# Kernel optimization log

Hardware: AMD Instinct MI355X
Metric: run time of the kernel (lower is better)

Reference implementation:

```python
import jax, jax.numpy as jnp
import numpy as np

def setup_inputs() -> dict:
    key = jax.random.key(0)
    k1, k2, k3, k4, k5 = jax.random.split(key, 5)
    vocab, embed, hidden = 32000, 1024, 1024
    batch, src_len = 64, 512
    src = jax.random.randint(k1, (batch, src_len), 0, vocab)
    emb_table = jax.random.normal(k2, (vocab, embed), dtype=jnp.float32)
    # xavier_uniform bounds
    bx = float(np.sqrt(6.0 / (embed + hidden)))
    bh = float(np.sqrt(6.0 / (hidden + hidden)))
    W_xh = jax.random.uniform(k3, (hidden, embed), minval=-bx, maxval=bx, dtype=jnp.float32)
    b_xh = jax.random.uniform(k4, (hidden,), minval=-1.0/np.sqrt(embed), maxval=1.0/np.sqrt(embed), dtype=jnp.float32)
    W_hh = jax.random.uniform(k5, (hidden, hidden), minval=-bh, maxval=bh, dtype=jnp.float32)
    return {"src": src, "emb_table": emb_table, "W_xh": W_xh, "b_xh": b_xh, "W_hh": W_hh}

def reference(src, emb_table, W_xh, b_xh, W_hh):
    # embedded: (batch, src_len, embed)
    embedded = emb_table[src]
    # precompute input projection for all timesteps: (batch, src_len, hidden)
    x_proj = jnp.einsum('bte,he->bth', embedded, W_xh) + b_xh
    batch = src.shape[0]
    hidden = W_hh.shape[0]
    h0 = jnp.zeros((batch, hidden), dtype=jnp.float32)

    def step(h, x_t):
        h_new = jnp.tanh(x_t + h @ W_hh.T)
        return h_new, None

    # scan over time: x_proj transposed to (src_len, batch, hidden)
    h_final, _ = jax.lax.scan(step, h0, jnp.swapaxes(x_proj, 0, 1))
    return h_final
```

## Files before the change

### kernel.cpp

```cpp
#include <hip/hip_runtime.h>
#include <hip/hip_fp16.h>

typedef _Float16 half8 __attribute__((ext_vector_type(8)));
typedef float floatx4 __attribute__((ext_vector_type(4)));

#define HBUF_BYTES (2ull * 16 * 1024 * 8)
#define CTL_BYTES  (32ull * 1024)
#define XP_OFF     (HBUF_BYTES + CTL_BYTES)
#define XP_BYTES   (512ull * 64 * 1024 * 2)
#define FLAG_STRIDE 16

union pack4 { unsigned long long u; _Float16 h[4]; };

__device__ inline half8 cvt8(const float4 a, const float4 b) {
    half8 r;
    r[0] = (_Float16)a.x; r[1] = (_Float16)a.y; r[2] = (_Float16)a.z; r[3] = (_Float16)a.w;
    r[4] = (_Float16)b.x; r[5] = (_Float16)b.y; r[6] = (_Float16)b.z; r[7] = (_Float16)b.w;
    return r;
}

__global__ __launch_bounds__(256) void xproj_kernel(
    const int* __restrict__ src, const float* __restrict__ emb,
    const float* __restrict__ Wxh, const float* __restrict__ bxh,
    _Float16* __restrict__ xp)
{
    __shared__ _Float16 As[128][40];
    __shared__ _Float16 Bs[128][40];

    const int tid  = threadIdx.x;
    const int lane = tid & 63;
    const int w    = tid >> 6;
    const int m15  = lane & 15;
    const int quad = lane >> 4;
    const int bid  = blockIdx.x;
    const int bn   = bid & 7;
    const int bm   = bid >> 3;
    const int m0   = bm * 128, n0 = bn * 128;
    const int wm   = w & 1, wn = w >> 1;

    const int  srow = tid >> 1;
    const int  scol = (tid & 1) * 16;
    const long arow = (long)src[m0 + srow] * 1024;
    const float* abase = emb + arow + scol;
    const float* bbase = Wxh + (long)(n0 + srow) * 1024 + scol;

    floatx4 zero4 = {0.f, 0.f, 0.f, 0.f};
    floatx4 acc[4][4];
#pragma unroll
    for (int mt = 0; mt < 4; mt++)
#pragma unroll
        for (int nt = 0; nt < 4; nt++) acc[mt][nt] = zero4;

    for (int k0 = 0; k0 < 1024; k0 += 32) {
        __syncthreads();
        float4 a0 = *(const float4*)(abase + k0);
        float4 a1 = *(const float4*)(abase + k0 + 4);
        float4 a2 = *(const float4*)(abase + k0 + 8);
        float4 a3 = *(const float4*)(abase + k0 + 12);
        float4 b0 = *(const float4*)(bbase + k0);
        float4 b1 = *(const float4*)(bbase + k0 + 4);
        float4 b2 = *(const float4*)(bbase + k0 + 8);
        float4 b3 = *(const float4*)(bbase + k0 + 12);
        *(half8*)&As[srow][scol]     = cvt8(a0, a1);
        *(half8*)&As[srow][scol + 8] = cvt8(a2, a3);
        *(half8*)&Bs[srow][scol]     = cvt8(b0, b1);
        *(half8*)&Bs[srow][scol + 8] = cvt8(b2, b3);
        __syncthreads();

        half8 af[4], bf[4];
#pragma unroll
        for (int mt = 0; mt < 4; mt++)
            af[mt] = *(const half8*)&As[wm * 64 + mt * 16 + m15][quad * 8];
#pragma unroll
        for (int nt = 0; nt < 4; nt++)
            bf[nt] = *(const half8*)&Bs[wn * 64 + nt * 16 + m15][quad * 8];
#pragma unroll
        for (int mt = 0; mt < 4; mt++)
#pragma unroll
            for (int nt = 0; nt < 4; nt++)
                acc[mt][nt] = __builtin_amdgcn_mfma_f32_16x16x32_f16(
                    af[mt], bf[nt], acc[mt][nt], 0, 0, 0);
    }

#pragma unroll
    for (int nt = 0; nt < 4; nt++) {
        const int n = n0 + wn * 64 + nt * 16 + m15;
        const float bias = bxh[n];
#pragma unroll
        for (int mt = 0; mt < 4; mt++) {
            const int mrow = m0 + wm * 64 + mt * 16 + quad * 4;
#pragma unroll
            for (int r = 0; r < 4; r++) {
                const int m = mrow + r;
                const int b = m >> 9;
                const int t = m & 511;
                xp[((long)t * 64 + b) * 1024 + n] = (_Float16)(acc[mt][nt][r] + bias);
            }
        }
    }
}

__global__ __launch_bounds__(256, 1) void rnn_kernel(
    const float* __restrict__ Whh, const _Float16* __restrict__ xp,
    unsigned long long* __restrict__ hb, int* __restrict__ flags,
    float* __restrict__ out)
{
    __shared__ _Float16 hstage[16][1032];
    __shared__ floatx4  cred[4][4][64];

    const int tid    = threadIdx.x;
    const int lane   = tid & 63;
    const int w      = tid >> 6;
    const int m15    = lane & 15;
    const int quad   = lane >> 4;
    const int wg     = blockIdx.x;
    const int g      = wg & 15;
    const int member = wg >> 4;
    const int b0     = g * 4;

    for (int i = tid; i < 16 * 1032; i += 256) ((_Float16*)hstage)[i] = (_Float16)0.f;

    half8 Wf[4][8];
#pragma unroll
    for (int nt = 0; nt < 4; nt++) {
        const float* wrow = Whh + (long)(member * 64 + nt * 16 + m15) * 1024
                                + w * 256 + quad * 8;
#pragma unroll
        for (int kk = 0; kk < 8; kk++) {
            float4 lo = *(const float4*)(wrow + kk * 32);
            float4 hi = *(const float4*)(wrow + kk * 32 + 4);
            Wf[nt][kk] = cvt8(lo, hi);
        }
    }
    __syncthreads();

    const int dim = member * 64 + w * 16 + m15;
    float xv[4] = {0.f, 0.f, 0.f, 0.f};
    if (quad == 0) {
#pragma unroll
        for (int r = 0; r < 4; r++)
            xv[r] = (float)xp[((long)0 * 64 + b0 + r) * 1024 + dim];
    }

    int* myflag = flags + (g * 16 + member) * FLAG_STRIDE;
    const int* gflags = flags + g * 16 * FLAG_STRIDE;
    floatx4 zero4 = {0.f, 0.f, 0.f, 0.f};

    for (int t = 0; t < 512; t++) {
        const unsigned long long* hcu = hb + (size_t)(t & 1) * 16384 + (size_t)g * 1024;
        unsigned long long*       hnu = hb + (size_t)((t + 1) & 1) * 16384 + (size_t)g * 1024;

        if (t > 0) {
            if (tid < 16) {
                const int* fw = gflags + tid * FLAG_STRIDE;
                while (__hip_atomic_load(fw, __ATOMIC_RELAXED,
                                         __HIP_MEMORY_SCOPE_AGENT) < t) { }
            }
            __syncthreads();
        }

        {
            unsigned long long v[4];
#pragma unroll
            for (int i = 0; i < 4; i++)
                v[i] = __hip_atomic_load(hcu + tid + 256 * i, __ATOMIC_RELAXED,
                                         __HIP_MEMORY_SCOPE_AGENT);
#pragma unroll
            for (int i = 0; i < 4; i++) {
                pack4 p; p.u = v[i];
                const int d = tid + 256 * i;
#pragma unroll
                for (int b = 0; b < 4; b++) hstage[b][d] = p.h[b];
            }
        }
        __syncthreads();

        floatx4 pacc[4];
#pragma unroll
        for (int nt = 0; nt < 4; nt++) pacc[nt] = zero4;
#pragma unroll
        for (int kk = 0; kk < 8; kk++) {
            half8 a = *(const half8*)&hstage[m15][w * 256 + kk * 32 + quad * 8];
#pragma unroll
            for (int nt = 0; nt < 4; nt++)
                pacc[nt] = __builtin_amdgcn_mfma_f32_16x16x32_f16(
                    a, Wf[nt][kk], pacc[nt], 0, 0, 0);
        }

#pragma unroll
        for (int nt = 0; nt < 4; nt++) cred[w][nt][lane] = pacc[nt];
        __syncthreads();
        floatx4 dsum = cred[0][w][lane];
#pragma unroll
        for (int ww = 1; ww < 4; ww++) dsum += cred[ww][w][lane];

        if (quad == 0) {
            pack4 p;
#pragma unroll
            for (int r = 0; r < 4; r++) {
                float pre  = dsum[r] + xv[r];
                float e    = __expf(2.0f * pre);
                float hval = 1.0f - 2.0f / (e + 1.0f);
                p.h[r] = (_Float16)hval;
                if (t == 511) out[(b0 + r) * 1024 + dim] = hval;
            }
            __hip_atomic_store(hnu + dim, p.u, __ATOMIC_RELAXED,
                               __HIP_MEMORY_SCOPE_AGENT);
        }

        __syncthreads();
        if (tid == 0)
            __hip_atomic_store(myflag, t + 1, __ATOMIC_RELAXED,
                               __HIP_MEMORY_SCOPE_AGENT);

        if (t < 511 && quad == 0) {
#pragma unroll
            for (int r = 0; r < 4; r++)
                xv[r] = (float)xp[((long)(t + 1) * 64 + b0 + r) * 1024 + dim];
        }
    }
}

extern "C" void kernel_launch(void* const* d_in, const int* in_sizes, int n_in,
                              void* d_out, int out_size, void* d_ws, size_t ws_size,
                              hipStream_t stream) {
    const int*   src = (const int*)d_in[0];
    const float* emb = (const float*)d_in[1];
    const float* Wxh = (const float*)d_in[2];
    const float* bxh = (const float*)d_in[3];
    const float* Whh = (const float*)d_in[4];
    float* out = (float*)d_out;

    char* ws = (char*)d_ws;
    unsigned long long* hb = (unsigned long long*)ws;
    int* flags = (int*)(ws + HBUF_BYTES);
    _Float16* xp = (_Float16*)(ws + XP_OFF);

    hipMemsetAsync(ws, 0, HBUF_BYTES + CTL_BYTES, stream);

    hipLaunchKernelGGL(xproj_kernel, dim3(2048), dim3(256), 0, stream,
                       src, emb, Wxh, bxh, xp);

    hipLaunchKernelGGL(rnn_kernel, dim3(256), dim3(256), 0, stream,
                       Whh, xp, hb, flags, out);
}
```

Measured before the change: 1.309 ms.

## Replace per-step flag barrier with parity-tagged hidden-state polling

The separate flag array and its spin-wait plus store handshake are removed. Consumers now spin directly on the hidden-state words until a parity tag, kept in bit 14, matches the expected step. Bit 14 is the top fp16 exponent bit of the first packed element, which is always zero for tanh outputs. This drops one global round trip and two __syncthreads per timestep from the serial recurrence. In exchange, every thread polls global memory, and correctness now depends on the tag bit never being set by real hidden values.

Measured after the change: 1.197 ms. -8.5%, faster.

```diff
diff --git a/kernel.cpp b/kernel.cpp
--- a/kernel.cpp
+++ b/kernel.cpp
@@ -8,7 +8,8 @@
 #define CTL_BYTES  (32ull * 1024)
 #define XP_OFF     (HBUF_BYTES + CTL_BYTES)
 #define XP_BYTES   (512ull * 64 * 1024 * 2)
-#define FLAG_STRIDE 16
+
+#define TAG_BIT    (1ull << 14)
 
 union pack4 { unsigned long long u; _Float16 h[4]; };
 
@@ -102,8 +103,7 @@
 
 __global__ __launch_bounds__(256, 1) void rnn_kernel(
     const float* __restrict__ Whh, const _Float16* __restrict__ xp,
-    unsigned long long* __restrict__ hb, int* __restrict__ flags,
-    float* __restrict__ out)
+    unsigned long long* __restrict__ hb, float* __restrict__ out)
 {
     __shared__ _Float16 hstage[16][1032];
     __shared__ floatx4  cred[4][4][64];
@@ -142,36 +142,31 @@
             xv[r] = (float)xp[((long)0 * 64 + b0 + r) * 1024 + dim];
     }
 
-    int* myflag = flags + (g * 16 + member) * FLAG_STRIDE;
-    const int* gflags = flags + g * 16 * FLAG_STRIDE;
     floatx4 zero4 = {0.f, 0.f, 0.f, 0.f};
 
     for (int t = 0; t < 512; t++) {
         const unsigned long long* hcu = hb + (size_t)(t & 1) * 16384 + (size_t)g * 1024;
         unsigned long long*       hnu = hb + (size_t)((t + 1) & 1) * 16384 + (size_t)g * 1024;
-
-        if (t > 0) {
-            if (tid < 16) {
-                const int* fw = gflags + tid * FLAG_STRIDE;
-                while (__hip_atomic_load(fw, __ATOMIC_RELAXED,
-                                         __HIP_MEMORY_SCOPE_AGENT) < t) { }
-            }
-            __syncthreads();
-        }
-
-        {
-            unsigned long long v[4];
+        const unsigned long long exp_tag = (unsigned long long)(((t + 1) >> 1) & 1) << 14;
+
+        unsigned long long v[4];
+        for (;;) {
+            bool ok = true;
 #pragma unroll
             for (int i = 0; i < 4; i++)
                 v[i] = __hip_atomic_load(hcu + tid + 256 * i, __ATOMIC_RELAXED,
                                          __HIP_MEMORY_SCOPE_AGENT);
 #pragma unroll
-            for (int i = 0; i < 4; i++) {
-                pack4 p; p.u = v[i];
-                const int d = tid + 256 * i;
-#pragma unroll
-                for (int b = 0; b < 4; b++) hstage[b][d] = p.h[b];
-            }
+            for (int i = 0; i < 4; i++)
+                ok &= ((v[i] & TAG_BIT) == exp_tag);
+            if (ok) break;
+        }
+#pragma unroll
+        for (int i = 0; i < 4; i++) {
+            pack4 p; p.u = v[i] & ~TAG_BIT;
+            const int d = tid + 256 * i;
+#pragma unroll
+            for (int b = 0; b < 4; b++) hstage[b][d] = p.h[b];
         }
         __syncthreads();
 
@@ -204,14 +199,13 @@
                 p.h[r] = (_Float16)hval;
                 if (t == 511) out[(b0 + r) * 1024 + dim] = hval;
             }
-            __hip_atomic_store(hnu + dim, p.u, __ATOMIC_RELAXED,
-                               __HIP_MEMORY_SCOPE_AGENT);
-        }
-
-        __syncthreads();
-        if (tid == 0)
-            __hip_atomic_store(myflag, t + 1, __ATOMIC_RELAXED,
-                               __HIP_MEMORY_SCOPE_AGENT);
+            if (t < 511) {
+                const unsigned long long st_tag =
+                    (unsigned long long)(((t + 2) >> 1) & 1) << 14;
+                __hip_atomic_store(hnu + dim, p.u | st_tag, __ATOMIC_RELAXED,
+                                   __HIP_MEMORY_SCOPE_AGENT);
+            }
+        }
 
         if (t < 511 && quad == 0) {
 #pragma unroll
@@ -233,14 +227,13 @@
 
     char* ws = (char*)d_ws;
     unsigned long long* hb = (unsigned long long*)ws;
-    int* flags = (int*)(ws + HBUF_BYTES);
     _Float16* xp = (_Float16*)(ws + XP_OFF);
 
-    hipMemsetAsync(ws, 0, HBUF_BYTES + CTL_BYTES, stream);
+    hipMemsetAsync(ws, 0, HBUF_BYTES, stream);
 
     hipLaunchKernelGGL(xproj_kernel, dim3(2048), dim3(256), 0, stream,
                        src, emb, Wxh, bxh, xp);
 
     hipLaunchKernelGGL(rnn_kernel, dim3(256), dim3(256), 0, stream,
-                       Whh, xp, hb, flags, out);
-}
+                       Whh, xp, hb, out);
+}
```
